# Optimization experiments

Hardware: AMD Instinct MI355X
Metric: run time of the kernel (lower is better)

The kernel has to match this reference:

```python
import jax, jax.numpy as jnp
import numpy as np

N = 100000      # nodes
E = 1600000     # edges (avg degree 16)
IN = 256        # input feature dim
HID = 64        # per-head hidden dim
H = 4           # attention heads
FC = 256        # collator dim (= H*HID here)
OUT = 4         # classes
ALPHA = 0.2     # LeakyReLU slope


def setup_inputs() -> dict:
    key = jax.random.key(0)
    ks = jax.random.split(key, 24)

    def rn(k, shape, fan_in):
        return jax.random.normal(k, shape, jnp.float32) / np.sqrt(fan_in).astype(np.float32)

    x = jax.random.normal(ks[0], (N, IN), jnp.float32)
    # ensure every node appears at least once as a source so the softmax denom is nonzero
    src = jnp.concatenate([jnp.arange(N, dtype=jnp.int32),
                           jax.random.randint(ks[1], (E - N,), 0, N, dtype=jnp.int32)])
    dst = jax.random.randint(ks[2], (E,), 0, N, dtype=jnp.int32)
    edge_index = jnp.stack([src, dst], axis=0)  # [2, E]

    # layer 1 heads (conv1d k=1 == linear): W [H, HID, IN]; a_1/a_2 conv -> vectors + scalar bias
    W1 = rn(ks[3], (H, HID, IN), IN)
    a11_w = rn(ks[4], (H, HID), HID); a11_b = jnp.zeros((H,), jnp.float32)
    a12_w = rn(ks[5], (H, HID), HID); a12_b = jnp.zeros((H,), jnp.float32)
    b1 = jnp.zeros((H, HID), jnp.float32)
    # layer 2 heads: input is H*HID
    W2 = rn(ks[6], (H, HID, H * HID), H * HID)
    a21_w = rn(ks[7], (H, HID), HID); a21_b = jnp.zeros((H,), jnp.float32)
    a22_w = rn(ks[8], (H, HID), HID); a22_b = jnp.zeros((H,), jnp.float32)
    b2 = jnp.zeros((H, HID), jnp.float32)
    # collator + classifier
    Wc = rn(ks[9], (FC, H * HID), H * HID); bc = jnp.zeros((FC,), jnp.float32)
    Wcls = rn(ks[10], (OUT, FC), FC); bcls = jnp.zeros((OUT,), jnp.float32)

    return dict(x=x, edge_index=edge_index,
                W1=W1, a11_w=a11_w, a11_b=a11_b, a12_w=a12_w, a12_b=a12_b, b1=b1,
                W2=W2, a21_w=a21_w, a21_b=a21_b, a22_w=a22_w, a22_b=a22_b, b2=b2,
                Wc=Wc, bc=bc, Wcls=Wcls, bcls=bcls)


def _gat_head(x, src, dst, W, a1w, a1b, a2w, a2b, b):
    h = x @ W.T                              # [N, HID]
    a1 = h @ a1w + a1b                       # [N] per-node src score
    a2 = h @ a2w + a2b                       # [N] per-node dst score
    s = jnp.exp(jax.nn.leaky_relu(a1[src] + a2[dst], ALPHA))   # [E]
    denom = jax.ops.segment_sum(s, src, num_segments=N)        # [N]
    agg = jax.ops.segment_sum(s[:, None] * h[dst], src, num_segments=N)  # [N, HID]
    return agg / denom[:, None] + b


def reference(x, edge_index, W1, a11_w, a11_b, a12_w, a12_b, b1,
              W2, a21_w, a21_b, a22_w, a22_b, b2, Wc, bc, Wcls, bcls):
    src, dst = edge_index[0], edge_index[1]
    h1 = jnp.concatenate(
        [_gat_head(x, src, dst, W1[i], a11_w[i], a11_b[i], a12_w[i], a12_b[i], b1[i])
         for i in range(H)], axis=1)         # [N, H*HID]
    h1 = jax.nn.relu(h1)
    h2 = jnp.concatenate(
        [_gat_head(h1, src, dst, W2[i], a21_w[i], a21_b[i], a22_w[i], a22_b[i], b2[i])
         for i in range(H)], axis=1)         # [N, H*HID]
    feat = jax.nn.relu(h2 @ Wc.T + bc)       # [N, FC]
    return feat @ Wcls.T + bcls              # [N, OUT]
```

## Files before the change

### kernel.cpp

```cpp
#include <hip/hip_runtime.h>
#include <hip/hip_bf16.h>
#include <hip/hip_fp16.h>
#include <stdint.h>

#define H 4
#define HID 64
#define CDIM 256
#define OUTC 4
#define ALPHA 0.2f
#define NW 16
#define MAXB 512
#define TILE1 4096

typedef __attribute__((ext_vector_type(8))) _Float16 f16x8;
typedef __attribute__((ext_vector_type(4))) float f32x4;

#define GLOBAL_AS(p) ((const __attribute__((address_space(1))) void*)(p))
#define LDS_AS(p)    ((__attribute__((address_space(3))) void*)(p))

__global__ void detect_k(const uint32_t* __restrict__ xw, int* __restrict__ flag) {
    __shared__ int sd[256];
    int t = threadIdx.x;
    int hits = 0;
    for (int i = 0; i < 16; ++i) {
        uint32_t w = xw[t * 16 + i];
        uint32_t ex = (w >> 7) & 0xffu;
        if (ex >= 100u && ex <= 145u) hits++;
    }
    sd[t] = hits;
    __syncthreads();
    for (int s = 128; s > 0; s >>= 1) {
        if (t < s) sd[t] += sd[t + s];
        __syncthreads();
    }
    if (t == 0) *flag = (sd[0] > 3000) ? 1 : 0;
}

struct WPtrs {
    const void* p[NW];
    int sz[NW];
    int off[NW];
};

__global__ void convert_k(WPtrs ptrs, float* __restrict__ outf, __half* __restrict__ outh,
                          const int* __restrict__ flag) {
    int which = blockIdx.y;
    int n = ptrs.sz[which];
    int i = blockIdx.x * 256 + threadIdx.x;
    if (i >= n) return;
    float v;
    if (*flag) v = __bfloat162float(((const __hip_bfloat16*)ptrs.p[which])[i]);
    else       v = ((const float*)ptrs.p[which])[i];
    outf[ptrs.off[which] + i] = v;
    outh[ptrs.off[which] + i] = __float2half(v);
}

__global__ __launch_bounds__(512) void bhist_k(const int* __restrict__ srcI,
                                               int* __restrict__ bucketCnt,
                                               int Ee, int nbuck)
{
    __shared__ int bc[MAXB];
    int t = threadIdx.x;
    bc[t] = 0;
    __syncthreads();
    int base = blockIdx.x * TILE1;
    #pragma unroll
    for (int q = 0; q < 8; ++q) {
        int i = base + q * 512 + t;
        if (i < Ee) atomicAdd(&bc[srcI[i] >> 8], 1);
    }
    __syncthreads();
    if (t < nbuck && bc[t] > 0) atomicAdd(&bucketCnt[t], bc[t]);
}

__global__ __launch_bounds__(512) void bscan_k(
    const int* __restrict__ bucketCnt, int* __restrict__ bucketCur,
    int* __restrict__ bucketStart, int* __restrict__ rowStart,
    int nbuck, int Nn, int Ee)
{
    __shared__ int sd[MAXB];
    int t = threadIdx.x;
    int v = (t < nbuck) ? bucketCnt[t] : 0;
    sd[t] = v;
    __syncthreads();
    for (int off = 1; off < MAXB; off <<= 1) {
        int add = (t >= off) ? sd[t - off] : 0;
        __syncthreads();
        sd[t] += add;
        __syncthreads();
    }
    if (t < nbuck) {
        int excl = sd[t] - v;
        bucketCur[t] = excl;
        bucketStart[t] = excl;
    }
    if (t == 0) { bucketStart[nbuck] = Ee; rowStart[Nn] = Ee; }
}

__global__ __launch_bounds__(512) void pass1_k(
    const int* __restrict__ srcI, const int* __restrict__ dstI,
    int* __restrict__ bucketCur, uint32_t* __restrict__ pairs,
    int Ee, int nbuck)
{
    __shared__ int cntL[MAXB], scanL[MAXB], exclL[MAXB], curL[MAXB], gbaseL[MAXB];
    __shared__ uint32_t sortedV[TILE1];
    __shared__ uint16_t sortedB[TILE1];
    const int t = threadIdx.x;
    const int base = blockIdx.x * TILE1;
    cntL[t] = 0;
    __syncthreads();
    uint32_t vq[8]; int bq[8];
    #pragma unroll
    for (int q = 0; q < 8; ++q) {
        int i = base + q * 512 + t;
        if (i < Ee) {
            int s = srcI[i], d = dstI[i];
            bq[q] = s >> 8;
            vq[q] = ((uint32_t)d << 8) | (uint32_t)(s & 255);
            atomicAdd(&cntL[bq[q]], 1);
        } else bq[q] = -1;
    }
    __syncthreads();
    scanL[t] = cntL[t];
    __syncthreads();
    for (int off = 1; off < MAXB; off <<= 1) {
        int add = (t >= off) ? scanL[t - off] : 0;
        __syncthreads();
        scanL[t] += add;
        __syncthreads();
    }
    int excl = scanL[t] - cntL[t];
    exclL[t] = excl;
    curL[t] = excl;
    if (t < nbuck && cntL[t] > 0)
        gbaseL[t] = atomicAdd(&bucketCur[t], cntL[t]);
    __syncthreads();
    #pragma unroll
    for (int q = 0; q < 8; ++q) {
        if (bq[q] >= 0) {
            int pos = atomicAdd(&curL[bq[q]], 1);
            sortedV[pos] = vq[q];
            sortedB[pos] = (uint16_t)bq[q];
        }
    }
    __syncthreads();
    int tcount = min(TILE1, Ee - base);
    for (int j = t; j < tcount; j += 512) {
        int b = sortedB[j];
        pairs[gbaseL[b] + (j - exclL[b])] = sortedV[j];
    }
}

__global__ __launch_bounds__(256) void pass2_k(
    const uint32_t* __restrict__ pairs, const int* __restrict__ bucketStart,
    int* __restrict__ rowStart, int* __restrict__ colI, int Nn)
{
    __shared__ int ncnt[256], sd[256], lcur[256];
    int b = blockIdx.x, t = threadIdx.x;
    int n0 = b << 8;
    int s = bucketStart[b], e = bucketStart[b + 1];
    ncnt[t] = 0;
    __syncthreads();
    for (int p = s + t; p < e; p += 256)
        atomicAdd(&ncnt[pairs[p] & 255], 1);
    __syncthreads();
    int v = ncnt[t];
    sd[t] = v;
    __syncthreads();
    for (int off = 1; off < 256; off <<= 1) {
        int add = (t >= off) ? sd[t - off] : 0;
        __syncthreads();
        sd[t] += add;
        __syncthreads();
    }
    int start = s + sd[t] - v;
    lcur[t] = start;
    if (n0 + t < Nn) rowStart[n0 + t] = start;
    __syncthreads();
    for (int p = s + t; p < e; p += 256) {
        uint32_t pv = pairs[p];
        int q = atomicAdd(&lcur[pv & 255], 1);
        colI[q] = (int)(pv >> 8);
    }
}

template <int AMODE, int OMODE>
__global__ __launch_bounds__(256) void gemm_k(
    const void* __restrict__ Ap, const __half* __restrict__ B,
    const float* __restrict__ bias, void* __restrict__ Cp, int M,
    const int* __restrict__ flagp,
    const float* __restrict__ a1w, const float* __restrict__ a1b,
    const float* __restrict__ a2w, const float* __restrict__ a2b,
    float* __restrict__ a1v, __half* __restrict__ a2v)
{
    __shared__ __align__(16) char smem[128 * 136 * 2];
    const int tid  = threadIdx.x;
    const int row0 = blockIdx.y * 128;
    const int col0 = blockIdx.x * 128;
    const int wave = tid >> 6, lane = tid & 63;
    const int m0w = (wave & 1) * 64;
    const int n0w = (wave >> 1) * 64;
    const int lm = lane & 15, lg = lane >> 4;
    const int isbf = (AMODE == 0) ? *flagp : 0;

    const __half* A = (const __half*)Ap;
    const int lrow = wave * 32 + (lane >> 2);
    const int kcL  = lane & 3;
    const size_t arow0 = (size_t)min(row0 + lrow,      M - 1) * CDIM;
    const size_t arow1 = (size_t)min(row0 + lrow + 16, M - 1) * CDIM;
    const size_t brow0 = (size_t)(col0 + lrow) * CDIM;
    const size_t brow1 = (size_t)(col0 + lrow + 16) * CDIM;

    f32x4 acc[4][4] = {};

    auto stageAB = [&](int buf, int k0) {
        char* Ab = smem + buf * 16384;
        char* Bb = Ab + 8192;
        if constexpr (AMODE == 1) {
            __builtin_amdgcn_global_load_lds(GLOBAL_AS(A + arow0 + k0 + kcL * 8),
                LDS_AS(Ab + wave * 2048), 16, 0, 0);
            __builtin_amdgcn_global_load_lds(GLOBAL_AS(A + arow1 + k0 + kcL * 8),
                LDS_AS(Ab + wave * 2048 + 1024), 16, 0, 0);
        } else {
            #pragma unroll
            for (int l = 0; l < 2; ++l) {
                int c = tid + l * 256;
                int m = c >> 2, kc = c & 3;
                int gr = row0 + m;
                uint4 q = make_uint4(0u, 0u, 0u, 0u);
                if (gr < M) {
                    __half hv[8];
                    if (isbf) {
                        const uint4 qb = *(const uint4*)((const __hip_bfloat16*)Ap
                                           + (size_t)gr * CDIM + k0 + kc * 8);
                        const uint32_t* w = (const uint32_t*)&qb;
                        #pragma unroll
                        for (int p = 0; p < 4; ++p) {
                            hv[2*p]   = __float2half(__uint_as_float((w[p] & 0xffffu) << 16));
                            hv[2*p+1] = __float2half(__uint_as_float(w[p] & 0xffff0000u));
                        }
                    } else {
                        const float* Af = (const float*)Ap + (size_t)gr * CDIM + k0 + kc * 8;
                        const float4 f0 = *(const float4*)Af;
                        const float4 f1 = *(const float4*)(Af + 4);
                        hv[0]=__float2half(f0.x); hv[1]=__float2half(f0.y);
                        hv[2]=__float2half(f0.z); hv[3]=__float2half(f0.w);
                        hv[4]=__float2half(f1.x); hv[5]=__float2half(f1.y);
                        hv[6]=__float2half(f1.z); hv[7]=__float2half(f1.w);
                    }
                    q = *(uint4*)hv;
                }
                *(uint4*)(Ab + m * 64 + kc * 16) = q;
            }
        }
        __builtin_amdgcn_global_load_lds(GLOBAL_AS(B + brow0 + k0 + kcL * 8),
            LDS_AS(Bb + wave * 2048), 16, 0, 0);
        __builtin_amdgcn_global_load_lds(GLOBAL_AS(B + brow1 + k0 + kcL * 8),
            LDS_AS(Bb + wave * 2048 + 1024), 16, 0, 0);
    };

    stageAB(0, 0);
    if constexpr (AMODE == 0) __syncthreads();
    int cur = 0;
    for (int kt = 0; kt < 8; ++kt) {
        if (kt < 7) stageAB(cur ^ 1, (kt + 1) * 32);
        if constexpr (AMODE == 1) {
            if (kt < 7) asm volatile("s_waitcnt vmcnt(4)" ::: "memory");
            else        asm volatile("s_waitcnt vmcnt(0)" ::: "memory");
            __builtin_amdgcn_s_barrier();
            asm volatile("" ::: "memory");
            __builtin_amdgcn_sched_barrier(0);
        } else {
            __syncthreads();
        }
        const char* Ab = smem + cur * 16384;
        const char* Bb = Ab + 8192;
        f16x8 af[4], bfr[4];
        #pragma unroll
        for (int i = 0; i < 4; ++i)
            af[i] = *(const f16x8*)(Ab + (m0w + i * 16 + lm) * 64 + lg * 16);
        #pragma unroll
        for (int j = 0; j < 4; ++j)
            bfr[j] = *(const f16x8*)(Bb + (n0w + j * 16 + lm) * 64 + lg * 16);
        #pragma unroll
        for (int i = 0; i < 4; ++i)
            #pragma unroll
            for (int j = 0; j < 4; ++j)
                acc[i][j] = __builtin_amdgcn_mfma_f32_16x16x32_f16(
                    af[i], bfr[j], acc[i][j], 0, 0, 0);
        if constexpr (AMODE == 1) {
            __builtin_amdgcn_sched_barrier(0);
            asm volatile("" ::: "memory");
            __builtin_amdgcn_s_barrier();
            asm volatile("" ::: "memory");
        } else {
            __syncthreads();
        }
        cur ^= 1;
    }

    if constexpr (OMODE == 1) {
        __half (*Cs)[136] = (__half(*)[136])smem;
        #pragma unroll
        for (int i = 0; i < 4; ++i)
            #pragma unroll
            for (int r = 0; r < 4; ++r) {
                int lr = m0w + i * 16 + lg * 4 + r;
                #pragma unroll
                for (int j = 0; j < 4; ++j)
                    Cs[lr][n0w + j * 16 + lm] = __float2half(acc[i][j][r]);
            }
        __syncthreads();
        __half* C = (__half*)Cp;
        #pragma unroll
        for (int l = 0; l < 8; ++l) {
            int c = tid + l * 256;
            int rr = c >> 4, cc = c & 15;
            int gr = row0 + rr;
            if (gr < M)
                *(uint4*)(C + (size_t)gr * CDIM + col0 + cc * 8) = *(uint4*)(&Cs[rr][cc * 8]);
        }
        {
            const int hsel = wave >> 1;
            const int ghead = (col0 >> 6) + hsel;
            float wv1[4], wv2[4];
            #pragma unroll
            for (int j = 0; j < 4; ++j) {
                wv1[j] = a1w[ghead * 64 + j * 16 + lm];
                wv2[j] = a2w[ghead * 64 + j * 16 + lm];
            }
            const float b1s = a1b[ghead], b2s = a2b[ghead];
            #pragma unroll
            for (int i = 0; i < 4; ++i)
                #pragma unroll
                for (int r = 0; r < 4; ++r) {
                    float p1 = 0.f, p2 = 0.f;
                    #pragma unroll
                    for (int j = 0; j < 4; ++j) {
                        float v = acc[i][j][r];
                        p1 = fmaf(v, wv1[j], p1);
                        p2 = fmaf(v, wv2[j], p2);
                    }
                    #pragma unroll
                    for (int m = 1; m < 16; m <<= 1) {
                        p1 += __shfl_xor(p1, m);
                        p2 += __shfl_xor(p2, m);
                    }
                    int gr = row0 + m0w + i * 16 + lg * 4 + r;
                    if (lm == 0 && gr < M) {
                        a1v[(size_t)gr * H + ghead] = p1 + b1s;
                        a2v[(size_t)gr * H + ghead] = __float2half(p2 + b2s);
                    }
                }
        }
    } else {
        const float* Wc4 = a1w;
        float* pcls = a1v;
        const int slot = blockIdx.x * 2 + (wave >> 1);
        float wv[OUTC][4];
        #pragma unroll
        for (int o = 0; o < OUTC; ++o)
            #pragma unroll
            for (int j = 0; j < 4; ++j)
                wv[o][j] = Wc4[o * CDIM + col0 + n0w + j * 16 + lm];
        #pragma unroll
        for (int i = 0; i < 4; ++i)
            #pragma unroll
            for (int r = 0; r < 4; ++r) {
                int grow = row0 + m0w + i * 16 + lg * 4 + r;
                if (grow < M) {
                    float po[OUTC] = {0.f, 0.f, 0.f, 0.f};
                    #pragma unroll
                    for (int j = 0; j < 4; ++j) {
                        int gcol = col0 + n0w + j * 16 + lm;
                        float t = fmaxf(acc[i][j][r] + bias[gcol], 0.f);
                        #pragma unroll
                        for (int o = 0; o < OUTC; ++o)
                            po[o] = fmaf(t, wv[o][j], po[o]);
                    }
                    #pragma unroll
                    for (int m = 1; m < 16; m <<= 1)
                        #pragma unroll
                        for (int o = 0; o < OUTC; ++o)
                            po[o] += __shfl_xor(po[o], m);
                    if (lm < OUTC) {
                        float v = (lm == 0) ? po[0] : (lm == 1) ? po[1]
                                : (lm == 2) ? po[2] : po[3];
                        pcls[((size_t)grow * 4 + slot) * OUTC + lm] = v;
                    }
                }
            }
        (void)Cp;
    }
}

__global__ __launch_bounds__(256) void agg_k(
    const __half* __restrict__ h,
    const float* __restrict__ a1v, const __half* __restrict__ a2v,
    const int* __restrict__ rowStart, const int* __restrict__ colI,
    const float* __restrict__ bias, __half* __restrict__ outp, int relu, int Nn)
{
    int tid = threadIdx.x;
    int wave = tid >> 6, lane = tid & 63;
    int n = blockIdx.x * 4 + wave;
    if (n >= Nn) return;
    int head = lane >> 4;
    int s = rowStart[n], e = rowStart[n + 1];
    float ac0 = 0.f, ac1 = 0.f, ac2 = 0.f, ac3 = 0.f, den = 0.f;
    const __half* hl = h + lane * 4;
    const float a1n = a1v[(size_t)n * H + head];

    for (int p0 = s; p0 < e; p0 += 8) {
        const int cnt = e - p0;
        int d[8]; float a2q[8]; ushort4 u[8];
        #pragma unroll
        for (int q = 0; q < 8; ++q) {
            int p = p0 + ((q < cnt) ? q : 0);
            d[q] = colI[p];
        }
        #pragma unroll
        for (int q = 0; q < 8; ++q) {
            u[q] = *(const ushort4*)(hl + (size_t)d[q] * CDIM);
            a2q[q] = __half2float(a2v[(size_t)d[q] * H + head]);
        }
        #pragma unroll
        for (int q = 0; q < 8; ++q) {
            float z = a1n + a2q[q];
            z = (z > 0.f) ? z : ALPHA * z;
            float svq = (q < cnt) ? __expf(z) : 0.f;
            den += svq;
            ac0 = fmaf(svq, __half2float(__ushort_as_half(u[q].x)), ac0);
            ac1 = fmaf(svq, __half2float(__ushort_as_half(u[q].y)), ac1);
            ac2 = fmaf(svq, __half2float(__ushort_as_half(u[q].z)), ac2);
            ac3 = fmaf(svq, __half2float(__ushort_as_half(u[q].w)), ac3);
        }
    }

    den = (den > 0.f) ? den : 1.f;
    const float4 b4 = *(const float4*)(bias + lane * 4);
    float r0 = ac0 / den + b4.x;
    float r1 = ac1 / den + b4.y;
    float r2 = ac2 / den + b4.z;
    float r3 = ac3 / den + b4.w;
    if (relu) {
        r0 = fmaxf(r0, 0.f); r1 = fmaxf(r1, 0.f);
        r2 = fmaxf(r2, 0.f); r3 = fmaxf(r3, 0.f);
    }
    ushort4 o;
    o.x = __half_as_ushort(__float2half(r0));
    o.y = __half_as_ushort(__float2half(r1));
    o.z = __half_as_ushort(__float2half(r2));
    o.w = __half_as_ushort(__float2half(r3));
    *(ushort4*)(outp + (size_t)n * CDIM + lane * 4) = o;
}

__global__ void cls2_k(const float* __restrict__ pcls, const float* __restrict__ bcls,
                       void* __restrict__ out, int Nn, const int* __restrict__ flagp)
{
    int n = blockIdx.x * 256 + threadIdx.x;
    if (n >= Nn) return;
    const float4 p0 = *(const float4*)(pcls + (size_t)n * 16);
    const float4 p1 = *(const float4*)(pcls + (size_t)n * 16 + 4);
    const float4 p2 = *(const float4*)(pcls + (size_t)n * 16 + 8);
    const float4 p3 = *(const float4*)(pcls + (size_t)n * 16 + 12);
    float r0 = p0.x + p1.x + p2.x + p3.x + bcls[0];
    float r1 = p0.y + p1.y + p2.y + p3.y + bcls[1];
    float r2 = p0.z + p1.z + p2.z + p3.z + bcls[2];
    float r3 = p0.w + p1.w + p2.w + p3.w + bcls[3];
    if (*flagp) {
        __hip_bfloat16* o = (__hip_bfloat16*)out + (size_t)n * OUTC;
        o[0] = __float2bfloat16(r0); o[1] = __float2bfloat16(r1);
        o[2] = __float2bfloat16(r2); o[3] = __float2bfloat16(r3);
    } else {
        float* o = (float*)out + (size_t)n * OUTC;
        o[0] = r0; o[1] = r1; o[2] = r2; o[3] = r3;
    }
}

extern "C" void kernel_launch(void* const* d_in, const int* in_sizes, int n_in,
                              void* d_out, int out_size, void* d_ws, size_t ws_size,
                              hipStream_t stream)
{
    const void* x  = d_in[0];
    const int*  ei = (const int*)d_in[1];

    const int Nn = in_sizes[0] / CDIM;
    const int Ee = in_sizes[1] / 2;
    const int* srcI = ei;
    const int* dstI = ei + Ee;

    char* wsp = (char*)d_ws;
    size_t off = 0;
    auto alloc = [&](size_t bytes) -> void* {
        void* p = wsp + off;
        off += (bytes + 255) & ~(size_t)255;
        return p;
    };
    __half* hA   = (__half*)alloc((size_t)Nn * CDIM * 2);
    __half* hB   = (__half*)alloc((size_t)Nn * CDIM * 2);
    float*  a1v       = (float*)alloc((size_t)Nn * H * 4);
    __half* a2h       = (__half*)alloc((size_t)Nn * H * 2);
    float*  pcls      = (float*)alloc((size_t)Nn * 4 * OUTC * 4);
    int*    rowStart  = (int*)alloc((size_t)(Nn + 1) * 4);
    int*    colI      = (int*)alloc((size_t)Ee * 4);
    uint32_t* pairs   = (uint32_t*)alloc((size_t)Ee * 4);
    int*    bucketCnt   = (int*)alloc(MAXB * 4);
    int*    bucketCur   = (int*)alloc(MAXB * 4);
    int*    bucketStart = (int*)alloc((MAXB + 1) * 4);
    int*    flag      = (int*)alloc(256);
    float*  wconv     = (float*)alloc((size_t)200000 * 4);
    __half* wh        = (__half*)alloc((size_t)200000 * 2);
    (void)ws_size; (void)n_in; (void)out_size;

    detect_k<<<1, 256, 0, stream>>>((const uint32_t*)x, flag);
    WPtrs wp;
    int woff = 0;
    for (int i = 0; i < NW; ++i) {
        wp.p[i] = d_in[2 + i];
        wp.sz[i] = in_sizes[2 + i];
        wp.off[i] = woff;
        woff += in_sizes[2 + i];
    }
    {
        dim3 cgrid(256, NW);
        convert_k<<<cgrid, 256, 0, stream>>>(wp, wconv, wh, flag);
    }
    const float*  a11wf = wconv + wp.off[1];
    const float*  a11bf = wconv + wp.off[2];
    const float*  a12wf = wconv + wp.off[3];
    const float*  a12bf = wconv + wp.off[4];
    const float*  b1f   = wconv + wp.off[5];
    const float*  a21wf = wconv + wp.off[7];
    const float*  a21bf = wconv + wp.off[8];
    const float*  a22wf = wconv + wp.off[9];
    const float*  a22bf = wconv + wp.off[10];
    const float*  b2f   = wconv + wp.off[11];
    const float*  bcf   = wconv + wp.off[13];
    const float*  Wclsf = wconv + wp.off[14];
    const float*  bclsf = wconv + wp.off[15];
    const __half* W1h   = wh + wp.off[0];
    const __half* W2h   = wh + wp.off[6];
    const __half* Wch   = wh + wp.off[12];

    const int NB = (Nn + 255) / 256;
    const int NBUCK = (Nn + 255) >> 8;
    const int TB = (Ee + TILE1 - 1) / TILE1;

    hipMemsetAsync(bucketCnt, 0, MAXB * 4, stream);
    bhist_k<<<TB, 512, 0, stream>>>(srcI, bucketCnt, Ee, NBUCK);
    bscan_k<<<1, 512, 0, stream>>>(bucketCnt, bucketCur, bucketStart, rowStart,
                                   NBUCK, Nn, Ee);
    pass1_k<<<TB, 512, 0, stream>>>(srcI, dstI, bucketCur, pairs, Ee, NBUCK);
    pass2_k<<<NBUCK, 256, 0, stream>>>(pairs, bucketStart, rowStart, colI, Nn);

    dim3 ggrid(CDIM / 128, (Nn + 127) / 128);
    const int AB = (Nn + 3) / 4;

    gemm_k<0, 1><<<ggrid, 256, 0, stream>>>(x, W1h, nullptr, hA, Nn, flag,
                                            a11wf, a11bf, a12wf, a12bf, a1v, a2h);
    agg_k<<<AB, 256, 0, stream>>>(hA, a1v, a2h, rowStart, colI, b1f, hB, 1, Nn);

    gemm_k<1, 1><<<ggrid, 256, 0, stream>>>(hB, W2h, nullptr, hA, Nn, flag,
                                            a21wf, a21bf, a22wf, a22bf, a1v, a2h);
    agg_k<<<AB, 256, 0, stream>>>(hA, a1v, a2h, rowStart, colI, b2f, hB, 0, Nn);

    gemm_k<1, 0><<<ggrid, 256, 0, stream>>>(hB, Wch, bcf, nullptr, Nn, flag,
                                            Wclsf, nullptr, nullptr, nullptr,
                                            pcls, nullptr);
    cls2_k<<<NB, 256, 0, stream>>>(pcls, bclsf, d_out, Nn, flag);
}
```

Measured before the change: 621.7 us.

## Store hidden features in 32-column slabs and split aggregation per slab

Intermediate hidden features are now stored as eight column slabs of 32 halves (64 bytes per row) instead of row-major 256-wide rows. The GEMM epilogue writes into that layout, and the GEMM A-loads read contiguous slab chunks. The aggregation kernel launches one wave per node per slab, with 16 edges processed in parallel across lanes, each lane reading 16 bytes, followed by a shuffle reduction. The goal is for each gather touch a small contiguous 64-byte slab row, giving better cache locality per pass and more parallelism over edges. The cost is eight times as many aggregation blocks, each re-reading colI and a2v, plus the shuffle-reduction overhead.

```diff
diff --git a/kernel.cpp b/kernel.cpp
--- a/kernel.cpp
+++ b/kernel.cpp
@@ -203,23 +203,27 @@
     const int lm = lane & 15, lg = lane >> 4;
     const int isbf = (AMODE == 0) ? *flagp : 0;
 
-    const __half* A = (const __half*)Ap;
+    const char* A = (const char*)Ap;
     const int lrow = wave * 32 + (lane >> 2);
     const int kcL  = lane & 3;
-    const size_t arow0 = (size_t)min(row0 + lrow,      M - 1) * CDIM;
-    const size_t arow1 = (size_t)min(row0 + lrow + 16, M - 1) * CDIM;
     const size_t brow0 = (size_t)(col0 + lrow) * CDIM;
     const size_t brow1 = (size_t)(col0 + lrow + 16) * CDIM;
+    const int aoff0 = row0 * 64 + wave * 2048 + lane * 16;
+    const int amax  = M * 64 - 16;
 
     f32x4 acc[4][4] = {};
 
-    auto stageAB = [&](int buf, int k0) {
+    auto stageAB = [&](int buf, int kt) {
         char* Ab = smem + buf * 16384;
         char* Bb = Ab + 8192;
+        const int k0 = kt * 32;
         if constexpr (AMODE == 1) {
-            __builtin_amdgcn_global_load_lds(GLOBAL_AS(A + arow0 + k0 + kcL * 8),
+            const size_t slab = (size_t)kt * M * 64;
+            __builtin_amdgcn_global_load_lds(
+                GLOBAL_AS(A + slab + min(aoff0, amax)),
                 LDS_AS(Ab + wave * 2048), 16, 0, 0);
-            __builtin_amdgcn_global_load_lds(GLOBAL_AS(A + arow1 + k0 + kcL * 8),
+            __builtin_amdgcn_global_load_lds(
+                GLOBAL_AS(A + slab + min(aoff0 + 1024, amax)),
                 LDS_AS(Ab + wave * 2048 + 1024), 16, 0, 0);
         } else {
             #pragma unroll
@@ -253,9 +257,9 @@
                 *(uint4*)(Ab + m * 64 + kc * 16) = q;
             }
         }
-        __builtin_amdgcn_global_load_lds(GLOBAL_AS(B + brow0 + k0 + kcL * 8),
+        __builtin_amdgcn_global_load_lds(GLOBAL_AS((const __half*)B + brow0 + k0 + kcL * 8),
             LDS_AS(Bb + wave * 2048), 16, 0, 0);
-        __builtin_amdgcn_global_load_lds(GLOBAL_AS(B + brow1 + k0 + kcL * 8),
+        __builtin_amdgcn_global_load_lds(GLOBAL_AS((const __half*)B + brow1 + k0 + kcL * 8),
             LDS_AS(Bb + wave * 2048 + 1024), 16, 0, 0);
     };
 
@@ -263,7 +267,7 @@
     if constexpr (AMODE == 0) __syncthreads();
     int cur = 0;
     for (int kt = 0; kt < 8; ++kt) {
-        if (kt < 7) stageAB(cur ^ 1, (kt + 1) * 32);
+        if (kt < 7) stageAB(cur ^ 1, kt + 1);
         if constexpr (AMODE == 1) {
             if (kt < 7) asm volatile("s_waitcnt vmcnt(4)" ::: "memory");
             else        asm volatile("s_waitcnt vmcnt(0)" ::: "memory");
@@ -311,14 +315,17 @@
                     Cs[lr][n0w + j * 16 + lm] = __float2half(acc[i][j][r]);
             }
         __syncthreads();
-        __half* C = (__half*)Cp;
+        char* C = (char*)Cp;
         #pragma unroll
         for (int l = 0; l < 8; ++l) {
             int c = tid + l * 256;
             int rr = c >> 4, cc = c & 15;
             int gr = row0 + rr;
-            if (gr < M)
-                *(uint4*)(C + (size_t)gr * CDIM + col0 + cc * 8) = *(uint4*)(&Cs[rr][cc * 8]);
+            if (gr < M) {
+                int q = (col0 >> 5) + (cc >> 2);
+                *(uint4*)(C + (size_t)q * M * 64 + (size_t)gr * 64 + (cc & 3) * 16)
+                    = *(uint4*)(&Cs[rr][cc * 8]);
+            }
         }
         {
             const int hsel = wave >> 1;
@@ -395,63 +402,77 @@
 }
 
 __global__ __launch_bounds__(256) void agg_k(
-    const __half* __restrict__ h,
+    const __half* __restrict__ hS,
     const float* __restrict__ a1v, const __half* __restrict__ a2v,
     const int* __restrict__ rowStart, const int* __restrict__ colI,
-    const float* __restrict__ bias, __half* __restrict__ outp, int relu, int Nn)
-{
-    int tid = threadIdx.x;
-    int wave = tid >> 6, lane = tid & 63;
-    int n = blockIdx.x * 4 + wave;
+    const float* __restrict__ bias, __half* __restrict__ outS, int relu, int Nn)
+{
+    const int tid = threadIdx.x;
+    const int wave = tid >> 6, lane = tid & 63;
+    const int s = blockIdx.x & 7;
+    const int n = (blockIdx.x >> 3) * 4 + wave;
     if (n >= Nn) return;
-    int head = lane >> 4;
-    int s = rowStart[n], e = rowStart[n + 1];
-    float ac0 = 0.f, ac1 = 0.f, ac2 = 0.f, ac3 = 0.f, den = 0.f;
-    const __half* hl = h + lane * 4;
+    const int head = s >> 1;
+    const int e = lane >> 2, c = lane & 3;
+    const size_t slab = (size_t)s * Nn * 32;
+    const __half* hsl = hS + slab;
     const float a1n = a1v[(size_t)n * H + head];
-
-    for (int p0 = s; p0 < e; p0 += 8) {
-        const int cnt = e - p0;
-        int d[8]; float a2q[8]; ushort4 u[8];
-        #pragma unroll
-        for (int q = 0; q < 8; ++q) {
-            int p = p0 + ((q < cnt) ? q : 0);
-            d[q] = colI[p];
-        }
-        #pragma unroll
-        for (int q = 0; q < 8; ++q) {
-            u[q] = *(const ushort4*)(hl + (size_t)d[q] * CDIM);
-            a2q[q] = __half2float(a2v[(size_t)d[q] * H + head]);
-        }
-        #pragma unroll
-        for (int q = 0; q < 8; ++q) {
-            float z = a1n + a2q[q];
-            z = (z > 0.f) ? z : ALPHA * z;
-            float svq = (q < cnt) ? __expf(z) : 0.f;
-            den += svq;
-            ac0 = fmaf(svq, __half2float(__ushort_as_half(u[q].x)), ac0);
-            ac1 = fmaf(svq, __half2float(__ushort_as_half(u[q].y)), ac1);
-            ac2 = fmaf(svq, __half2float(__ushort_as_half(u[q].z)), ac2);
-            ac3 = fmaf(svq, __half2float(__ushort_as_half(u[q].w)), ac3);
-        }
-    }
-
-    den = (den > 0.f) ? den : 1.f;
-    const float4 b4 = *(const float4*)(bias + lane * 4);
-    float r0 = ac0 / den + b4.x;
-    float r1 = ac1 / den + b4.y;
-    float r2 = ac2 / den + b4.z;
-    float r3 = ac3 / den + b4.w;
-    if (relu) {
-        r0 = fmaxf(r0, 0.f); r1 = fmaxf(r1, 0.f);
-        r2 = fmaxf(r2, 0.f); r3 = fmaxf(r3, 0.f);
-    }
-    ushort4 o;
-    o.x = __half_as_ushort(__float2half(r0));
-    o.y = __half_as_ushort(__float2half(r1));
-    o.z = __half_as_ushort(__float2half(r2));
-    o.w = __half_as_ushort(__float2half(r3));
-    *(ushort4*)(outp + (size_t)n * CDIM + lane * 4) = o;
+    const int p0 = rowStart[n], pe = rowStart[n + 1];
+
+    float f0=0.f,f1=0.f,f2=0.f,f3=0.f,f4=0.f,f5=0.f,f6=0.f,f7=0.f,den=0.f;
+    for (int base = p0; base < pe; base += 16) {
+        const int cnt = pe - base;
+        const int slot = base + ((e < cnt) ? e : 0);
+        const int d = colI[slot];
+        const uint4 u = *(const uint4*)(hsl + (size_t)d * 32 + c * 8);
+        const float a2q = __half2float(a2v[(size_t)d * H + head]);
+        float z = a1n + a2q;
+        z = (z > 0.f) ? z : ALPHA * z;
+        const float sv = (e < cnt) ? __expf(z) : 0.f;
+        den += sv;
+        f0 = fmaf(sv, __half2float(__ushort_as_half((ushort)(u.x & 0xffffu))), f0);
+        f1 = fmaf(sv, __half2float(__ushort_as_half((ushort)(u.x >> 16))),    f1);
+        f2 = fmaf(sv, __half2float(__ushort_as_half((ushort)(u.y & 0xffffu))), f2);
+        f3 = fmaf(sv, __half2float(__ushort_as_half((ushort)(u.y >> 16))),    f3);
+        f4 = fmaf(sv, __half2float(__ushort_as_half((ushort)(u.z & 0xffffu))), f4);
+        f5 = fmaf(sv, __half2float(__ushort_as_half((ushort)(u.z >> 16))),    f5);
+        f6 = fmaf(sv, __half2float(__ushort_as_half((ushort)(u.w & 0xffffu))), f6);
+        f7 = fmaf(sv, __half2float(__ushort_as_half((ushort)(u.w >> 16))),    f7);
+    }
+    #pragma unroll
+    for (int m = 4; m <= 32; m <<= 1) {
+        den += __shfl_xor(den, m);
+        f0 += __shfl_xor(f0, m); f1 += __shfl_xor(f1, m);
+        f2 += __shfl_xor(f2, m); f3 += __shfl_xor(f3, m);
+        f4 += __shfl_xor(f4, m); f5 += __shfl_xor(f5, m);
+        f6 += __shfl_xor(f6, m); f7 += __shfl_xor(f7, m);
+    }
+    if (e == 0) {
+        den = (den > 0.f) ? den : 1.f;
+        const float* bp = bias + s * 32 + c * 8;
+        const float4 b0 = *(const float4*)bp;
+        const float4 b1 = *(const float4*)(bp + 4);
+        float r0 = f0 / den + b0.x, r1 = f1 / den + b0.y;
+        float r2 = f2 / den + b0.z, r3 = f3 / den + b0.w;
+        float r4 = f4 / den + b1.x, r5 = f5 / den + b1.y;
+        float r6 = f6 / den + b1.z, r7 = f7 / den + b1.w;
+        if (relu) {
+            r0 = fmaxf(r0, 0.f); r1 = fmaxf(r1, 0.f);
+            r2 = fmaxf(r2, 0.f); r3 = fmaxf(r3, 0.f);
+            r4 = fmaxf(r4, 0.f); r5 = fmaxf(r5, 0.f);
+            r6 = fmaxf(r6, 0.f); r7 = fmaxf(r7, 0.f);
+        }
+        ushort o[8];
+        o[0] = __half_as_ushort(__float2half(r0));
+        o[1] = __half_as_ushort(__float2half(r1));
+        o[2] = __half_as_ushort(__float2half(r2));
+        o[3] = __half_as_ushort(__float2half(r3));
+        o[4] = __half_as_ushort(__float2half(r4));
+        o[5] = __half_as_ushort(__float2half(r5));
+        o[6] = __half_as_ushort(__float2half(r6));
+        o[7] = __half_as_ushort(__float2half(r7));
+        *(uint4*)(outS + slab + (size_t)n * 32 + c * 8) = *(uint4*)o;
+    }
 }
 
 __global__ void cls2_k(const float* __restrict__ pcls, const float* __restrict__ bcls,
@@ -554,15 +575,15 @@
     pass2_k<<<NBUCK, 256, 0, stream>>>(pairs, bucketStart, rowStart, colI, Nn);
 
     dim3 ggrid(CDIM / 128, (Nn + 127) / 128);
-    const int AB = (Nn + 3) / 4;
+    const int AB2 = ((Nn + 3) / 4) * 8;
 
     gemm_k<0, 1><<<ggrid, 256, 0, stream>>>(x, W1h, nullptr, hA, Nn, flag,
                                             a11wf, a11bf, a12wf, a12bf, a1v, a2h);
-    agg_k<<<AB, 256, 0, stream>>>(hA, a1v, a2h, rowStart, colI, b1f, hB, 1, Nn);
+    agg_k<<<AB2, 256, 0, stream>>>(hA, a1v, a2h, rowStart, colI, b1f, hB, 1, Nn);
 
     gemm_k<1, 1><<<ggrid, 256, 0, stream>>>(hB, W2h, nullptr, hA, Nn, flag,
                                             a21wf, a21bf, a22wf, a22bf, a1v, a2h);
-    agg_k<<<AB, 256, 0, stream>>>(hA, a1v, a2h, rowStart, colI, b2f, hB, 0, Nn);
+    agg_k<<<AB2, 256, 0, stream>>>(hA, a1v, a2h, rowStart, colI, b2f, hB, 0, Nn);
 
     gemm_k<1, 0><<<ggrid, 256, 0, stream>>>(hB, Wch, bcf, nullptr, Nn, flag,
                                             Wclsf, nullptr, nullptr, nullptr,
```

New measurement: 1.022 ms. +64.4%, slower.
